# Kernel optimization log

Measured on AMD Instinct MI355X. Metric: run time of the kernel, lower is better.

## Reference

```python
import jax, jax.numpy as jnp
import numpy as np

NEURONS = 54
DT = 4
STEPS = 30
POOL = 8


def setup_inputs() -> dict:
    key = jax.random.key(0)
    k1, k2, k3, k4 = jax.random.split(key, 4)
    B = 128
    x = jax.random.normal(k1, (B, 1, 600, 600), dtype=jnp.float32)
    # GLM history weights (torch.rand init; scaled down so exp(current_sum) stays finite)
    l_weight = jax.random.uniform(k2, (NEURONS, DT), dtype=jnp.float32) * 0.01
    h_weight = jax.random.uniform(k3, (DT,), dtype=jnp.float32) * 0.01
    fc_w = jax.random.normal(k4, (NEURONS, 75 * 75), dtype=jnp.float32) * 0.02
    fc_b = jnp.zeros((NEURONS,), dtype=jnp.float32)
    return {"x": x, "l_weight": l_weight, "h_weight": h_weight, "fc_w": fc_w, "fc_b": fc_b}


def _spike(rate):
    # LIF_sNeuron + SpikingNN: spike = (rate > mean(rate)); straight-through grad where rate > thr
    thr = jax.lax.stop_gradient(jnp.mean(rate))
    mask = rate > thr
    return mask.astype(rate.dtype) + jnp.where(mask, rate - jax.lax.stop_gradient(rate), 0.0)


def reference(x, l_weight, h_weight, fc_w, fc_b):
    B = x.shape[0]
    # avg_pool2d(x, 8): [B,1,600,600] -> [B,1,75,75]
    xp = x.reshape(B, 1, 75, POOL, 75, POOL).mean(axis=(3, 5))
    xf = xp.reshape(B, 75 * 75) @ fc_w.T + fc_b  # [B, 54]

    def step(carry, _):
        count, hist = carry  # [B,N], [B,N,DT]
        hs = hist * l_weight  # [B,N,DT]
        lateral = hs.sum(axis=(1, 2))[:, None] - hs.sum(axis=2)  # sum over other neurons
        cur = xf + lateral + (hist * h_weight).sum(axis=2)
        spike = _spike(jnp.exp(cur))
        hist = jnp.concatenate([hist[:, :, 1:], spike[:, :, None]], axis=2)
        return (count + spike, hist), None

    init = (jnp.zeros((B, NEURONS), x.dtype), jnp.zeros((B, NEURONS, DT), x.dtype))
    (count, _), _ = jax.lax.scan(step, init, None, length=STEPS)
    return jax.nn.softplus(count)
```

## Files before the change

kernel.cpp:

```cpp
#include <hip/hip_runtime.h>
#include <hip/hip_bf16.h>
#include <math.h>

#define BATCH 128
#define NEUR 54
#define DT 4
#define STEPS 30
#define PDIM 75
#define K (PDIM * PDIM)
#define K_PAD 5632
#define TOT (BATCH * NEUR)
#define RTPB 1024

#define POOL_BLOCKS ((BATCH * K_PAD) / 256)
#define TRANS_BLOCKS ((K_PAD * 64) / 256)

__global__ void prep_kernel(const float* __restrict__ x, const float* __restrict__ fc_w,
                            float* __restrict__ xp, float* __restrict__ fc_wt) {
    if (blockIdx.x < POOL_BLOCKS) {
        int o = blockIdx.x * 256 + threadIdx.x;
        int b = o / K_PAD;
        int rem = o - b * K_PAD;
        if (rem >= K) { xp[o] = 0.f; return; }
        int i = rem / PDIM;
        int j = rem - i * PDIM;
        const float* base = x + (size_t)b * 360000 + (size_t)(i * 8) * 600 + j * 8;
        float s = 0.f;
#pragma unroll
        for (int r = 0; r < 8; r++) {
            const float4* p4 = (const float4*)(base + r * 600);
            float4 a = p4[0];
            float4 c = p4[1];
            s += a.x + a.y + a.z + a.w + c.x + c.y + c.z + c.w;
        }
        xp[o] = s * (1.0f / 64.0f);
    } else {
        int o = (blockIdx.x - POOL_BLOCKS) * 256 + threadIdx.x;
        int k = o >> 6;
        int n = o & 63;
        float v = (n < NEUR && k < K) ? fc_w[(size_t)n * K + k] : 0.f;
        fc_wt[o] = v;
    }
}

__global__ __launch_bounds__(512) void fc_kernel(const float* __restrict__ xp,
                                                 const float* __restrict__ fc_wt,
                                                 const float* __restrict__ fc_b,
                                                 float* __restrict__ xf) {
    int b = blockIdx.x;
    int tid = threadIdx.x;
    int n = tid & 63;
    int kg = tid >> 6;
    const float* xr = xp + (size_t)b * K_PAD;
    float a0 = 0.f, a1 = 0.f, a2 = 0.f, a3 = 0.f;
    for (int k = kg; k < K_PAD; k += 32) {
        float x0 = xr[k];
        float x1 = xr[k + 8];
        float x2 = xr[k + 16];
        float x3 = xr[k + 24];
        a0 += x0 * fc_wt[(size_t)(k) * 64 + n];
        a1 += x1 * fc_wt[(size_t)(k + 8) * 64 + n];
        a2 += x2 * fc_wt[(size_t)(k + 16) * 64 + n];
        a3 += x3 * fc_wt[(size_t)(k + 24) * 64 + n];
    }
    float acc = (a0 + a1) + (a2 + a3);
    __shared__ float sred[8][64];
    sred[kg][n] = acc;
    __syncthreads();
    if (tid < 64) {
        float v = 0.f;
#pragma unroll
        for (int w = 0; w < 8; w++) v += sred[w][tid];
        if (tid < NEUR) xf[b * NEUR + tid] = v + fc_b[tid];
    }
}

__global__ __launch_bounds__(RTPB) void recurrence_kernel(const float* __restrict__ xf,
                                                          const float* __restrict__ l_weight,
                                                          const float* __restrict__ h_weight,
                                                          float* __restrict__ out) {
    __shared__ float red[2][16];

    int tid = threadIdx.x;
    int b = tid >> 3;
    int sub = tid & 7;
    int n0 = sub * 7;
    int cntn = NEUR - n0; if (cntn > 7) cntn = 7; if (cntn < 0) cntn = 0;

    float hw0 = h_weight[0], hw1 = h_weight[1], hw2 = h_weight[2], hw3 = h_weight[3];

    float hist[7][DT];
    float lw[7][DT];
    float xfv[7], cnt[7], rate[7];

#pragma unroll
    for (int j = 0; j < 7; j++) {
        cnt[j] = 0.f;
#pragma unroll
        for (int d = 0; d < DT; d++) hist[j][d] = 0.f;
        if (j < cntn) {
            int n = n0 + j;
            xfv[j] = xf[b * NEUR + n];
#pragma unroll
            for (int d = 0; d < DT; d++) lw[j][d] = l_weight[n * DT + d];
        } else {
            xfv[j] = 0.f;
#pragma unroll
            for (int d = 0; d < DT; d++) lw[j][d] = 0.f;
        }
    }

    int wid = tid >> 6;
    int lane = tid & 63;

    for (int s = 0; s < STEPS; s++) {
        float hsum[7];
        float btl = 0.f;
#pragma unroll
        for (int j = 0; j < 7; j++) {
            hsum[j] = hist[j][0] * lw[j][0] + hist[j][1] * lw[j][1] +
                      hist[j][2] * lw[j][2] + hist[j][3] * lw[j][3];
            btl += hsum[j];
        }
#pragma unroll
        for (int off = 4; off > 0; off >>= 1) btl += __shfl_xor(btl, off, 8);
        float lsum = 0.f;
#pragma unroll
        for (int j = 0; j < 7; j++) {
            if (j < cntn) {
                float hterm = hist[j][0] * hw0 + hist[j][1] * hw1 +
                              hist[j][2] * hw2 + hist[j][3] * hw3;
                float cur = xfv[j] + (btl - hsum[j]) + hterm;
                rate[j] = expf(cur);
                lsum += rate[j];
            }
        }
#pragma unroll
        for (int off = 32; off > 0; off >>= 1) lsum += __shfl_xor(lsum, off, 64);
        if (lane == 0) red[s & 1][wid] = lsum;
        __syncthreads();
        float tsum = 0.f;
#pragma unroll
        for (int w = 0; w < 16; w++) tsum += red[s & 1][w];
        float thr = tsum * (1.0f / (float)TOT);
#pragma unroll
        for (int j = 0; j < 7; j++) {
            if (j < cntn) {
                float sp = (rate[j] > thr) ? 1.0f : 0.0f;
                cnt[j] += sp;
                hist[j][0] = hist[j][1];
                hist[j][1] = hist[j][2];
                hist[j][2] = hist[j][3];
                hist[j][3] = sp;
            }
        }
    }

#pragma unroll
    for (int j = 0; j < 7; j++) {
        if (j < cntn) {
            float c = cnt[j];
            out[b * NEUR + n0 + j] = c + log1pf(expf(-c));
        }
    }
}

extern "C" void kernel_launch(void* const* d_in, const int* in_sizes, int n_in,
                              void* d_out, int out_size, void* d_ws, size_t ws_size,
                              hipStream_t stream) {
    const float* x = (const float*)d_in[0];
    const float* l_weight = (const float*)d_in[1];
    const float* h_weight = (const float*)d_in[2];
    const float* fc_w = (const float*)d_in[3];
    const float* fc_b = (const float*)d_in[4];
    float* out = (float*)d_out;

    float* xp = (float*)d_ws;
    float* fc_wt = xp + (size_t)BATCH * K_PAD;
    float* xf = fc_wt + (size_t)K_PAD * 64;

    prep_kernel<<<POOL_BLOCKS + TRANS_BLOCKS, 256, 0, stream>>>(x, fc_w, xp, fc_wt);
    fc_kernel<<<BATCH, 512, 0, stream>>>(xp, fc_wt, fc_b, xf);
    recurrence_kernel<<<1, RTPB, 0, stream>>>(xf, l_weight, h_weight, out);
}
```

Measured before the change: 381.8 us.

## Fuse avg-pool and FC into one kernel with split-K partial sums

Merges the pooling, weight-transpose and FC kernels into one kernel. Each of 256 blocks pools half of one batch row into shared memory and computes dot products against the untransposed fc_w rows. The two partial sums are added in the recurrence kernel together with the bias. This drops a kernel launch, the pooled-activation and transposed-weight round trips through global memory, and the transpose itself. The cost is that fc_w is reread by every block and only 256 blocks are launched to stream the large input. The recurrence threshold reduction also now reads shared memory with float4 loads.

```diff
diff --git a/kernel.cpp b/kernel.cpp
--- a/kernel.cpp
+++ b/kernel.cpp
@@ -8,74 +8,86 @@
 #define STEPS 30
 #define PDIM 75
 #define K (PDIM * PDIM)
-#define K_PAD 5632
+#define HALF 2816
 #define TOT (BATCH * NEUR)
 #define RTPB 1024
 
-#define POOL_BLOCKS ((BATCH * K_PAD) / 256)
-#define TRANS_BLOCKS ((K_PAD * 64) / 256)
+__global__ __launch_bounds__(1024) void poolfc_kernel(const float* __restrict__ x,
+                                                      const float* __restrict__ fc_w,
+                                                      float* __restrict__ xf_part) {
+    __shared__ float xps[HALF];
+    int blk = blockIdx.x;
+    int b = blk >> 1;
+    int h = blk & 1;
+    int tid = threadIdx.x;
+    int kbase = h * HALF;
+    int cnt = h ? (K - HALF) : HALF;
+    const float* xrow = x + (size_t)b * 360000;
 
-__global__ void prep_kernel(const float* __restrict__ x, const float* __restrict__ fc_w,
-                            float* __restrict__ xp, float* __restrict__ fc_wt) {
-    if (blockIdx.x < POOL_BLOCKS) {
-        int o = blockIdx.x * 256 + threadIdx.x;
-        int b = o / K_PAD;
-        int rem = o - b * K_PAD;
-        if (rem >= K) { xp[o] = 0.f; return; }
-        int i = rem / PDIM;
-        int j = rem - i * PDIM;
-        const float* base = x + (size_t)b * 360000 + (size_t)(i * 8) * 600 + j * 8;
+    for (int w = tid; w < HALF; w += 1024) {
         float s = 0.f;
+        if (w < cnt) {
+            int gw = kbase + w;
+            int i = gw / PDIM;
+            int j = gw - i * PDIM;
+            const float* base = xrow + (size_t)(i * 8) * 600 + j * 8;
 #pragma unroll
-        for (int r = 0; r < 8; r++) {
-            const float4* p4 = (const float4*)(base + r * 600);
-            float4 a = p4[0];
-            float4 c = p4[1];
-            s += a.x + a.y + a.z + a.w + c.x + c.y + c.z + c.w;
+            for (int r = 0; r < 8; r++) {
+                const float4* p4 = (const float4*)(base + r * 600);
+                float4 a = p4[0];
+                float4 c = p4[1];
+                s += a.x + a.y + a.z + a.w + c.x + c.y + c.z + c.w;
+            }
+            s *= (1.0f / 64.0f);
         }
-        xp[o] = s * (1.0f / 64.0f);
-    } else {
-        int o = (blockIdx.x - POOL_BLOCKS) * 256 + threadIdx.x;
-        int k = o >> 6;
-        int n = o & 63;
-        float v = (n < NEUR && k < K) ? fc_w[(size_t)n * K + k] : 0.f;
-        fc_wt[o] = v;
+        xps[w] = s;
+    }
+    __syncthreads();
+
+    int wid = tid >> 6, lane = tid & 63;
+    int nb = wid * 4;
+    if (nb < NEUR) {
+        int v1 = (nb + 1 < NEUR), v2 = (nb + 2 < NEUR), v3 = (nb + 3 < NEUR);
+        int n1 = v1 ? nb + 1 : nb;
+        int n2 = v2 ? nb + 2 : nb;
+        int n3 = v3 ? nb + 3 : nb;
+        const float* p0 = fc_w + (size_t)nb * K + kbase;
+        const float* p1 = fc_w + (size_t)n1 * K + kbase;
+        const float* p2 = fc_w + (size_t)n2 * K + kbase;
+        const float* p3 = fc_w + (size_t)n3 * K + kbase;
+        float a0 = 0.f, a1 = 0.f, a2 = 0.f, a3 = 0.f;
+        for (int c = 0; c < HALF / 64; c++) {
+            int kk = c * 64 + lane;
+            float xv = xps[kk];
+            bool inb = (kbase + kk) < K;
+            float f0 = inb ? p0[kk] : 0.f;
+            float f1 = inb ? p1[kk] : 0.f;
+            float f2 = inb ? p2[kk] : 0.f;
+            float f3 = inb ? p3[kk] : 0.f;
+            a0 += xv * f0;
+            a1 += xv * f1;
+            a2 += xv * f2;
+            a3 += xv * f3;
+        }
+#pragma unroll
+        for (int off = 32; off > 0; off >>= 1) {
+            a0 += __shfl_xor(a0, off, 64);
+            a1 += __shfl_xor(a1, off, 64);
+            a2 += __shfl_xor(a2, off, 64);
+            a3 += __shfl_xor(a3, off, 64);
+        }
+        if (lane == 0) {
+            float* dst = xf_part + (size_t)h * (BATCH * 64) + b * 64 + nb;
+            dst[0] = a0;
+            if (v1) dst[1] = a1;
+            if (v2) dst[2] = a2;
+            if (v3) dst[3] = a3;
+        }
     }
 }
 
-__global__ __launch_bounds__(512) void fc_kernel(const float* __restrict__ xp,
-                                                 const float* __restrict__ fc_wt,
-                                                 const float* __restrict__ fc_b,
-                                                 float* __restrict__ xf) {
-    int b = blockIdx.x;
-    int tid = threadIdx.x;
-    int n = tid & 63;
-    int kg = tid >> 6;
-    const float* xr = xp + (size_t)b * K_PAD;
-    float a0 = 0.f, a1 = 0.f, a2 = 0.f, a3 = 0.f;
-    for (int k = kg; k < K_PAD; k += 32) {
-        float x0 = xr[k];
-        float x1 = xr[k + 8];
-        float x2 = xr[k + 16];
-        float x3 = xr[k + 24];
-        a0 += x0 * fc_wt[(size_t)(k) * 64 + n];
-        a1 += x1 * fc_wt[(size_t)(k + 8) * 64 + n];
-        a2 += x2 * fc_wt[(size_t)(k + 16) * 64 + n];
-        a3 += x3 * fc_wt[(size_t)(k + 24) * 64 + n];
-    }
-    float acc = (a0 + a1) + (a2 + a3);
-    __shared__ float sred[8][64];
-    sred[kg][n] = acc;
-    __syncthreads();
-    if (tid < 64) {
-        float v = 0.f;
-#pragma unroll
-        for (int w = 0; w < 8; w++) v += sred[w][tid];
-        if (tid < NEUR) xf[b * NEUR + tid] = v + fc_b[tid];
-    }
-}
-
-__global__ __launch_bounds__(RTPB) void recurrence_kernel(const float* __restrict__ xf,
+__global__ __launch_bounds__(RTPB) void recurrence_kernel(const float* __restrict__ xf_part,
+                                                          const float* __restrict__ fc_b,
                                                           const float* __restrict__ l_weight,
                                                           const float* __restrict__ h_weight,
                                                           float* __restrict__ out) {
@@ -100,7 +112,7 @@
         for (int d = 0; d < DT; d++) hist[j][d] = 0.f;
         if (j < cntn) {
             int n = n0 + j;
-            xfv[j] = xf[b * NEUR + n];
+            xfv[j] = xf_part[b * 64 + n] + xf_part[BATCH * 64 + b * 64 + n] + fc_b[n];
 #pragma unroll
             for (int d = 0; d < DT; d++) lw[j][d] = l_weight[n * DT + d];
         } else {
@@ -139,9 +151,10 @@
         for (int off = 32; off > 0; off >>= 1) lsum += __shfl_xor(lsum, off, 64);
         if (lane == 0) red[s & 1][wid] = lsum;
         __syncthreads();
-        float tsum = 0.f;
-#pragma unroll
-        for (int w = 0; w < 16; w++) tsum += red[s & 1][w];
+        const float4* r4 = (const float4*)red[s & 1];
+        float4 q0 = r4[0], q1 = r4[1], q2 = r4[2], q3 = r4[3];
+        float tsum = ((q0.x + q0.y) + (q0.z + q0.w)) + ((q1.x + q1.y) + (q1.z + q1.w)) +
+                     ((q2.x + q2.y) + (q2.z + q2.w)) + ((q3.x + q3.y) + (q3.z + q3.w));
         float thr = tsum * (1.0f / (float)TOT);
 #pragma unroll
         for (int j = 0; j < 7; j++) {
@@ -175,11 +188,8 @@
     const float* fc_b = (const float*)d_in[4];
     float* out = (float*)d_out;
 
-    float* xp = (float*)d_ws;
-    float* fc_wt = xp + (size_t)BATCH * K_PAD;
-    float* xf = fc_wt + (size_t)K_PAD * 64;
+    float* xf_part = (float*)d_ws;
 
-    prep_kernel<<<POOL_BLOCKS + TRANS_BLOCKS, 256, 0, stream>>>(x, fc_w, xp, fc_wt);
-    fc_kernel<<<BATCH, 512, 0, stream>>>(xp, fc_wt, fc_b, xf);
-    recurrence_kernel<<<1, RTPB, 0, stream>>>(xf, l_weight, h_weight, out);
+    poolfc_kernel<<<BATCH * 2, 1024, 0, stream>>>(x, fc_w, xf_part);
+    recurrence_kernel<<<1, RTPB, 0, stream>>>(xf_part, fc_b, l_weight, h_weight, out);
 }
```

After: 345.1 us. -9.6%, faster.
